# Performance work log

Hardware: AMD Instinct MI355X
Metric: run time of the kernel (lower is better)

## Reference

```python
import jax, jax.numpy as jnp
import numpy as np

N_NODES = 100000
N_EDGES = 1600000
IN_DIM = 256
OUT_DIM = 128


def setup_inputs() -> dict:
    key = jax.random.key(0)
    k1, k2, k3, k4, k5 = jax.random.split(key, 5)
    inputs = jax.random.normal(k1, (N_NODES, IN_DIM), dtype=jnp.float32)
    # xavier_uniform with relu gain, as in the torch init
    gain = float(np.sqrt(2.0))
    limit = gain * float(np.sqrt(6.0 / (IN_DIM + OUT_DIM)))
    W = jax.random.uniform(k2, (IN_DIM, OUT_DIM), dtype=jnp.float32,
                           minval=-limit, maxval=limit)
    edge_src = jax.random.randint(k3, (N_EDGES,), 0, N_NODES, dtype=jnp.int32)
    edge_dst = jax.random.randint(k4, (N_EDGES,), 0, N_NODES, dtype=jnp.int32)
    edge_val = jax.random.uniform(k5, (N_EDGES,), dtype=jnp.float32)
    return {"inputs": inputs, "W": W, "edge_src": edge_src,
            "edge_dst": edge_dst, "edge_val": edge_val}


def reference(inputs, W, edge_src, edge_dst, edge_val):
    # x = inputs @ W  (dense GEMM)
    h = inputs @ W                                  # [N, OUT_DIM]
    # adj @ h  as SpMM over COO edges: out[d] += val * h[s]
    msg = edge_val[:, None] * h[edge_src]           # [E, OUT_DIM]
    agg = jax.ops.segment_sum(msg, edge_dst, num_segments=N_NODES)
    # act = ReLU, fused with SpMM output
    return jax.nn.relu(agg)
```

## Files before the change

### kernel.cpp

```cpp
#include <hip/hip_runtime.h>
#include <hip/hip_bf16.h>

#define N_NODES 100000
#define N_EDGES 1600000
#define IN_DIM  256
#define OUT_DIM 128

#define GEMM_ROWS   64
#define GEMM_BLOCKS ((N_NODES + GEMM_ROWS - 1) / GEMM_ROWS)

#define NBUCK   196
#define BSHIFT  9
#define BCAP    10240
#define BSTRIDE 16
#define EPB     2048
#define BIN_BLOCKS ((N_EDGES + EPB - 1) / EPB)

typedef __attribute__((ext_vector_type(8))) short bf16x8;
typedef __attribute__((ext_vector_type(4))) float f32x4;

__device__ __forceinline__ ushort f2bf(float f) {
    union { float f; unsigned u; } v; v.f = f;
    unsigned r = v.u + 0x7FFF + ((v.u >> 16) & 1);
    return (ushort)(r >> 16);
}
__device__ __forceinline__ float bflo(unsigned u) {
    union { unsigned u; float f; } v; v.u = u << 16; return v.f;
}
__device__ __forceinline__ float bfhi(unsigned u) {
    union { unsigned u; float f; } v; v.u = u & 0xFFFF0000u; return v.f;
}

__global__ __launch_bounds__(256) void pack_w(const float* __restrict__ W,
                                              ushort* __restrict__ Wp) {
    const int t = blockIdx.x * 256 + threadIdx.x;
    if (t >= 4096) return;
    const int kk = t >> 9, n = (t >> 6) & 7, l = t & 63;
    const int kbase = kk * 32 + (l >> 4) * 8;
    const int col   = n * 16 + (l & 15);
    ushort* o = Wp + (size_t)t * 8;
#pragma unroll
    for (int j = 0; j < 8; ++j)
        o[j] = f2bf(W[(size_t)(kbase + j) * OUT_DIM + col]);
}

__global__ __launch_bounds__(256) void gemm_coarse(const float* __restrict__ X,
                                                   const bf16x8* __restrict__ Bp,
                                                   ushort* __restrict__ H,
                                                   const int* __restrict__ esrc,
                                                   const int* __restrict__ edst,
                                                   const float* __restrict__ eval,
                                                   int* __restrict__ bcur,
                                                   int2* __restrict__ binned) {
    __shared__ ushort xt[GEMM_ROWS * IN_DIM];

    if (blockIdx.x >= GEMM_BLOCKS) {
        int* cnt   = (int*)xt;
        int* sbase = (int*)xt + 256;
        const int blk = blockIdx.x - GEMM_BLOCKS;
        const int cb  = blk * EPB;
        const int lim = (N_EDGES - cb < EPB) ? (N_EDGES - cb) : EPB;
        const int tid = threadIdx.x;

        if (tid < NBUCK) cnt[tid] = 0;
        __syncthreads();
        for (int i = tid; i < lim; i += 256)
            atomicAdd(&cnt[edst[cb + i] >> BSHIFT], 1);
        __syncthreads();
        if (tid < NBUCK) {
            const int c = cnt[tid];
            sbase[tid] = c ? atomicAdd(&bcur[tid * BSTRIDE], c) : 0;
            cnt[tid] = 0;
        }
        __syncthreads();
        for (int i = tid; i < lim; i += 256) {
            const int d  = edst[cb + i];
            const int bb = d >> BSHIFT;
            const int pos = sbase[bb] + atomicAdd(&cnt[bb], 1);
            if (pos < BCAP) {
                int2 rec;
                rec.x = esrc[cb + i] | ((d & 511) << 20);
                rec.y = __float_as_int(eval[cb + i]);
                binned[(size_t)bb * BCAP + pos] = rec;
            }
        }
        return;
    }

    const int row0 = blockIdx.x * GEMM_ROWS;
    const int tid  = threadIdx.x;

    float4 v[16];
#pragma unroll
    for (int it = 0; it < 16; ++it) {
        const int tr = it * 4 + (tid >> 6);
        int grow = row0 + tr; if (grow >= N_NODES) grow = N_NODES - 1;
        v[it] = *reinterpret_cast<const float4*>(X + (size_t)grow * IN_DIM + (tid & 63) * 4);
    }
#pragma unroll
    for (int it = 0; it < 16; ++it) {
        const int tr = it * 4 + (tid >> 6);
        const int tc = (tid & 63) * 4;
        ushort4 b4;
        b4.x = f2bf(v[it].x); b4.y = f2bf(v[it].y);
        b4.z = f2bf(v[it].z); b4.w = f2bf(v[it].w);
        const int byte = (tr * 512 + tc * 2) ^ ((tr & 7) << 4);
        *reinterpret_cast<ushort4*>((char*)xt + byte) = b4;
    }
    __syncthreads();

    const int lane = tid & 63;
    const int wid  = tid >> 6;
    const int wr   = wid >> 1;
    const int wc   = wid & 1;
    const int rlo  = lane & 15;
    const int kseg = lane >> 4;
    const int rl0  = wr * 32 + rlo;
    const int rl1  = rl0 + 16;
    const int rxor = (rlo & 7) << 4;

    f32x4 acc[2][4] = {};

    for (int kk = 0; kk < 8; ++kk) {
        const int cb2 = (kk * 64 + kseg * 16) ^ rxor;
        const bf16x8 A0 = *reinterpret_cast<const bf16x8*>((const char*)xt + rl0 * 512 + cb2);
        const bf16x8 A1 = *reinterpret_cast<const bf16x8*>((const char*)xt + rl1 * 512 + cb2);
        const bf16x8* bbase = Bp + (size_t)(kk * 8 + wc * 4) * 64 + lane;
#pragma unroll
        for (int n = 0; n < 4; ++n) {
            const bf16x8 Bf = bbase[(size_t)n * 64];
            acc[0][n] = __builtin_amdgcn_mfma_f32_16x16x32_bf16(A0, Bf, acc[0][n], 0, 0, 0);
            acc[1][n] = __builtin_amdgcn_mfma_f32_16x16x32_bf16(A1, Bf, acc[1][n], 0, 0, 0);
        }
    }

#pragma unroll
    for (int i = 0; i < 2; ++i) {
#pragma unroll
        for (int r = 0; r < 4; ++r) {
            const int row = row0 + wr * 32 + i * 16 + kseg * 4 + r;
            if (row < N_NODES) {
#pragma unroll
                for (int n = 0; n < 4; ++n)
                    H[(size_t)row * OUT_DIM + (wc * 4 + n) * 16 + rlo] = f2bf(acc[i][n][r]);
            }
        }
    }
}

__global__ __launch_bounds__(256) void scan_buckets(const int* __restrict__ bcur,
                                                    int* __restrict__ gbase) {
    __shared__ int ws[4];
    const int tid = threadIdx.x, lane = tid & 63, wid = tid >> 6;
    const int v = (tid < NBUCK) ? bcur[tid * BSTRIDE] : 0;
    int sv = v;
#pragma unroll
    for (int d = 1; d < 64; d <<= 1) {
        const int t = __shfl_up(sv, d, 64);
        if (lane >= d) sv += t;
    }
    if (lane == 63) ws[wid] = sv;
    __syncthreads();
    int wx = 0;
#pragma unroll
    for (int w = 0; w < 4; ++w) if (w < wid) wx += ws[w];
    if (tid < NBUCK) gbase[tid] = wx + sv - v;
}

__global__ __launch_bounds__(1024) void bin_fine(const int* __restrict__ bcur,
                                                 const int* __restrict__ gbase,
                                                 const int2* __restrict__ binned,
                                                 int* __restrict__ offsets,
                                                 int2* __restrict__ recs) {
    __shared__ int nh[512];
    __shared__ int cur[512];
    __shared__ int ws[4];
    const int b   = blockIdx.x;
    const int tid = threadIdx.x, lane = tid & 63, wid = tid >> 6;
    const int node0 = b << BSHIFT;
    int nn = N_NODES - node0; if (nn > 512) nn = 512;
    int size = bcur[b * BSTRIDE]; if (size > BCAP) size = BCAP;
    const int2* in = binned + (size_t)b * BCAP;
    const int base_out = gbase[b];

    if (tid < 512) nh[tid] = 0;
    __syncthreads();
    for (int k = tid; k < size; k += 1024)
        atomicAdd(&nh[(in[k].x >> 20) & 511], 1);
    __syncthreads();

    int a0 = 0, ts = 0, sv = 0;
    if (tid < 256) {
        a0 = nh[2 * tid];
        const int a1 = nh[2 * tid + 1];
        ts = a0 + a1;
        sv = ts;
#pragma unroll
        for (int d = 1; d < 64; d <<= 1) {
            const int t = __shfl_up(sv, d, 64);
            if (lane >= d) sv += t;
        }
        if (lane == 63) ws[wid] = sv;
    }
    __syncthreads();
    if (tid < 256) {
        int wx = 0;
#pragma unroll
        for (int w = 0; w < 4; ++w) if (w < wid) wx += ws[w];
        const int ex = wx + sv - ts;
        cur[2 * tid]     = base_out + ex;
        cur[2 * tid + 1] = base_out + ex + a0;
        if (2 * tid < nn)     offsets[node0 + 2 * tid]     = base_out + ex;
        if (2 * tid + 1 < nn) offsets[node0 + 2 * tid + 1] = base_out + ex + a0;
    }
    if (b == 0 && tid == 0) offsets[N_NODES] = N_EDGES;
    __syncthreads();

    for (int k = tid; k < size; k += 1024) {
        const int2 r = in[k];
        const int pos = atomicAdd(&cur[(r.x >> 20) & 511], 1);
        int2 o; o.x = r.x & 0xFFFFF; o.y = r.y;
        recs[pos] = o;
    }
}

__global__ __launch_bounds__(256) void spmm_pull(const ushort* __restrict__ H,
                                                 const int* __restrict__ offsets,
                                                 const int2* __restrict__ recs,
                                                 float* __restrict__ out) {
    const int tid   = threadIdx.x;
    const int lane  = tid & 63;
    const int g     = lane >> 4;
    const int c     = lane & 15;
    const int gwave = blockIdx.x * 4 + (tid >> 6);
    const int node  = gwave * 4 + g;
    if (node >= N_NODES) return;

    const int beg = offsets[node];
    const int end = offsets[node + 1];

    float a0 = 0.f, a1 = 0.f, a2 = 0.f, a3 = 0.f;
    float a4 = 0.f, a5 = 0.f, a6 = 0.f, a7 = 0.f;

    int e = beg;
    for (; e + 3 < end; e += 4) {
        const int2 r0 = recs[e + 0];
        const int2 r1 = recs[e + 1];
        const int2 r2 = recs[e + 2];
        const int2 r3 = recs[e + 3];
        const uint4 h0 = *((const uint4*)(H + (size_t)r0.x * OUT_DIM) + c);
        const uint4 h1 = *((const uint4*)(H + (size_t)r1.x * OUT_DIM) + c);
        const uint4 h2 = *((const uint4*)(H + (size_t)r2.x * OUT_DIM) + c);
        const uint4 h3 = *((const uint4*)(H + (size_t)r3.x * OUT_DIM) + c);
        const float v0 = __int_as_float(r0.y), v1 = __int_as_float(r1.y);
        const float v2 = __int_as_float(r2.y), v3 = __int_as_float(r3.y);
        a0 = fmaf(v0, bflo(h0.x), a0);  a1 = fmaf(v0, bfhi(h0.x), a1);
        a2 = fmaf(v0, bflo(h0.y), a2);  a3 = fmaf(v0, bfhi(h0.y), a3);
        a4 = fmaf(v0, bflo(h0.z), a4);  a5 = fmaf(v0, bfhi(h0.z), a5);
        a6 = fmaf(v0, bflo(h0.w), a6);  a7 = fmaf(v0, bfhi(h0.w), a7);
        a0 = fmaf(v1, bflo(h1.x), a0);  a1 = fmaf(v1, bfhi(h1.x), a1);
        a2 = fmaf(v1, bflo(h1.y), a2);  a3 = fmaf(v1, bfhi(h1.y), a3);
        a4 = fmaf(v1, bflo(h1.z), a4);  a5 = fmaf(v1, bfhi(h1.z), a5);
        a6 = fmaf(v1, bflo(h1.w), a6);  a7 = fmaf(v1, bfhi(h1.w), a7);
        a0 = fmaf(v2, bflo(h2.x), a0);  a1 = fmaf(v2, bfhi(h2.x), a1);
        a2 = fmaf(v2, bflo(h2.y), a2);  a3 = fmaf(v2, bfhi(h2.y), a3);
        a4 = fmaf(v2, bflo(h2.z), a4);  a5 = fmaf(v2, bfhi(h2.z), a5);
        a6 = fmaf(v2, bflo(h2.w), a6);  a7 = fmaf(v2, bfhi(h2.w), a7);
        a0 = fmaf(v3, bflo(h3.x), a0);  a1 = fmaf(v3, bfhi(h3.x), a1);
        a2 = fmaf(v3, bflo(h3.y), a2);  a3 = fmaf(v3, bfhi(h3.y), a3);
        a4 = fmaf(v3, bflo(h3.z), a4);  a5 = fmaf(v3, bfhi(h3.z), a5);
        a6 = fmaf(v3, bflo(h3.w), a6);  a7 = fmaf(v3, bfhi(h3.w), a7);
    }
    for (; e < end; ++e) {
        const int2 r0 = recs[e];
        const float v0 = __int_as_float(r0.y);
        const uint4 h0 = *((const uint4*)(H + (size_t)r0.x * OUT_DIM) + c);
        a0 = fmaf(v0, bflo(h0.x), a0);  a1 = fmaf(v0, bfhi(h0.x), a1);
        a2 = fmaf(v0, bflo(h0.y), a2);  a3 = fmaf(v0, bfhi(h0.y), a3);
        a4 = fmaf(v0, bflo(h0.z), a4);  a5 = fmaf(v0, bfhi(h0.z), a5);
        a6 = fmaf(v0, bflo(h0.w), a6);  a7 = fmaf(v0, bfhi(h0.w), a7);
    }

    float* op = out + (size_t)node * OUT_DIM + c * 8;
    float4 o0, o1;
    o0.x = fmaxf(a0, 0.f); o0.y = fmaxf(a1, 0.f);
    o0.z = fmaxf(a2, 0.f); o0.w = fmaxf(a3, 0.f);
    o1.x = fmaxf(a4, 0.f); o1.y = fmaxf(a5, 0.f);
    o1.z = fmaxf(a6, 0.f); o1.w = fmaxf(a7, 0.f);
    *reinterpret_cast<float4*>(op)     = o0;
    *reinterpret_cast<float4*>(op + 4) = o1;
}

extern "C" void kernel_launch(void* const* d_in, const int* in_sizes, int n_in,
                              void* d_out, int out_size, void* d_ws, size_t ws_size,
                              hipStream_t stream) {
    const float* X    = (const float*)d_in[0];
    const float* W    = (const float*)d_in[1];
    const int*   esrc = (const int*)d_in[2];
    const int*   edst = (const int*)d_in[3];
    const float* eval = (const float*)d_in[4];
    float*       out  = (float*)d_out;

    char* ws = (char*)d_ws;
    ushort* Hb     = (ushort*)ws;  ws += (size_t)N_NODES * OUT_DIM * sizeof(ushort);
    ushort* Wp     = (ushort*)ws;  ws += (size_t)4096 * 8 * sizeof(ushort);
    int*    offsets= (int*)ws;     ws += (((size_t)(N_NODES + 1) * 4 + 127) & ~(size_t)127);
    int*    bcur   = (int*)ws;     ws += (size_t)NBUCK * BSTRIDE * 4;
    int*    gbase  = (int*)ws;     ws += ((NBUCK * 4 + 127) & ~127);
    int2*   binned = (int2*)ws;    ws += (size_t)NBUCK * BCAP * sizeof(int2);
    int2*   recs   = (int2*)ws;

    pack_w<<<16, 256, 0, stream>>>(W, Wp);
    hipMemsetAsync(bcur, 0, (size_t)NBUCK * BSTRIDE * 4, stream);
    gemm_coarse<<<GEMM_BLOCKS + BIN_BLOCKS, 256, 0, stream>>>(X, (const bf16x8*)Wp, Hb,
                                                              esrc, edst, eval,
                                                              bcur, binned);

    scan_buckets<<<1, 256, 0, stream>>>(bcur, gbase);
    bin_fine<<<NBUCK, 1024, 0, stream>>>(bcur, gbase, binned, offsets, recs);

    spmm_pull<<<(N_NODES + 15) / 16, 256, 0, stream>>>(Hb, offsets, recs, out);
}
```

Before: 134.2 us.

## Load GEMM input tiles directly into LDS with smaller 16-row blocks

The GEMM phase now uses 16-row tiles instead of 64, copying fp32 X rows straight into swizzled LDS via global_load_lds. The per-element bf16 conversion moves to fragment-read time, and each wave computes a 16x32 output slice. Launch bounds request higher occupancy to hide the latency of the memory-bound X stream. The trade is re-reading W fragments from global or cache four times as often, which also shifts the binning blocks' index range. Dropping the tail guard relies on N_NODES being divisible by 16.

```diff
diff --git a/kernel.cpp b/kernel.cpp
--- a/kernel.cpp
+++ b/kernel.cpp
@@ -6,8 +6,8 @@
 #define IN_DIM  256
 #define OUT_DIM 128
 
-#define GEMM_ROWS   64
-#define GEMM_BLOCKS ((N_NODES + GEMM_ROWS - 1) / GEMM_ROWS)
+#define GEMM_ROWS   16
+#define GEMM_BLOCKS (N_NODES / GEMM_ROWS)
 
 #define NBUCK   196
 #define BSHIFT  9
@@ -44,15 +44,19 @@
         o[j] = f2bf(W[(size_t)(kbase + j) * OUT_DIM + col]);
 }
 
-__global__ __launch_bounds__(256) void gemm_coarse(const float* __restrict__ X,
-                                                   const bf16x8* __restrict__ Bp,
-                                                   ushort* __restrict__ H,
-                                                   const int* __restrict__ esrc,
-                                                   const int* __restrict__ edst,
-                                                   const float* __restrict__ eval,
-                                                   int* __restrict__ bcur,
-                                                   int2* __restrict__ binned) {
-    __shared__ ushort xt[GEMM_ROWS * IN_DIM];
+__global__ __launch_bounds__(256, 8) void gemm_coarse(const float* __restrict__ X,
+                                                      const bf16x8* __restrict__ Bp,
+                                                      ushort* __restrict__ H,
+                                                      const int* __restrict__ esrc,
+                                                      const int* __restrict__ edst,
+                                                      const float* __restrict__ eval,
+                                                      int* __restrict__ bcur,
+                                                      int2* __restrict__ binned) {
+    __shared__ float xt[GEMM_ROWS * IN_DIM];
+
+    const int tid  = threadIdx.x;
+    const int lane = tid & 63;
+    const int wid  = tid >> 6;
 
     if (blockIdx.x >= GEMM_BLOCKS) {
         int* cnt   = (int*)xt;
@@ -60,7 +64,6 @@
         const int blk = blockIdx.x - GEMM_BLOCKS;
         const int cb  = blk * EPB;
         const int lim = (N_EDGES - cb < EPB) ? (N_EDGES - cb) : EPB;
-        const int tid = threadIdx.x;
 
         if (tid < NBUCK) cnt[tid] = 0;
         __syncthreads();
@@ -88,64 +91,45 @@
     }
 
     const int row0 = blockIdx.x * GEMM_ROWS;
-    const int tid  = threadIdx.x;
-
-    float4 v[16];
-#pragma unroll
-    for (int it = 0; it < 16; ++it) {
-        const int tr = it * 4 + (tid >> 6);
-        int grow = row0 + tr; if (grow >= N_NODES) grow = N_NODES - 1;
-        v[it] = *reinterpret_cast<const float4*>(X + (size_t)grow * IN_DIM + (tid & 63) * 4);
-    }
-#pragma unroll
-    for (int it = 0; it < 16; ++it) {
-        const int tr = it * 4 + (tid >> 6);
-        const int tc = (tid & 63) * 4;
-        ushort4 b4;
-        b4.x = f2bf(v[it].x); b4.y = f2bf(v[it].y);
-        b4.z = f2bf(v[it].z); b4.w = f2bf(v[it].w);
-        const int byte = (tr * 512 + tc * 2) ^ ((tr & 7) << 4);
-        *reinterpret_cast<ushort4*>((char*)xt + byte) = b4;
-    }
-    __syncthreads();
-
-    const int lane = tid & 63;
-    const int wid  = tid >> 6;
-    const int wr   = wid >> 1;
-    const int wc   = wid & 1;
+
+#pragma unroll
+    for (int i = 0; i < 4; ++i) {
+        const int row  = wid * 4 + i;
+        const int grow = row0 + row;
+        const float* gp = X + (size_t)grow * IN_DIM
+                        + (((lane * 16) ^ ((row & 7) << 4)) >> 2);
+        __builtin_amdgcn_global_load_lds(
+            (const __attribute__((address_space(1))) void*)gp,
+            (__attribute__((address_space(3))) void*)&xt[row * IN_DIM], 16, 0, 0);
+    }
+    __syncthreads();
+
     const int rlo  = lane & 15;
     const int kseg = lane >> 4;
-    const int rl0  = wr * 32 + rlo;
-    const int rl1  = rl0 + 16;
-    const int rxor = (rlo & 7) << 4;
-
-    f32x4 acc[2][4] = {};
-
+    const int sw   = (rlo & 7) << 4;
+
+    f32x4 acc[2] = {};
+    const char* rp = (const char*)xt + rlo * 1024;
+
+#pragma unroll
     for (int kk = 0; kk < 8; ++kk) {
-        const int cb2 = (kk * 64 + kseg * 16) ^ rxor;
-        const bf16x8 A0 = *reinterpret_cast<const bf16x8*>((const char*)xt + rl0 * 512 + cb2);
-        const bf16x8 A1 = *reinterpret_cast<const bf16x8*>((const char*)xt + rl1 * 512 + cb2);
-        const bf16x8* bbase = Bp + (size_t)(kk * 8 + wc * 4) * 64 + lane;
-#pragma unroll
-        for (int n = 0; n < 4; ++n) {
-            const bf16x8 Bf = bbase[(size_t)n * 64];
-            acc[0][n] = __builtin_amdgcn_mfma_f32_16x16x32_bf16(A0, Bf, acc[0][n], 0, 0, 0);
-            acc[1][n] = __builtin_amdgcn_mfma_f32_16x16x32_bf16(A1, Bf, acc[1][n], 0, 0, 0);
-        }
-    }
-
-#pragma unroll
-    for (int i = 0; i < 2; ++i) {
-#pragma unroll
-        for (int r = 0; r < 4; ++r) {
-            const int row = row0 + wr * 32 + i * 16 + kseg * 4 + r;
-            if (row < N_NODES) {
-#pragma unroll
-                for (int n = 0; n < 4; ++n)
-                    H[(size_t)row * OUT_DIM + (wc * 4 + n) * 16 + rlo] = f2bf(acc[i][n][r]);
-            }
-        }
-    }
+        const int base = kk * 128 + kseg * 32;
+        const float4 alo = *(const float4*)(rp + (base ^ sw));
+        const float4 ahi = *(const float4*)(rp + ((base + 16) ^ sw));
+        bf16x8 A;
+        A[0]=f2bf(alo.x); A[1]=f2bf(alo.y); A[2]=f2bf(alo.z); A[3]=f2bf(alo.w);
+        A[4]=f2bf(ahi.x); A[5]=f2bf(ahi.y); A[6]=f2bf(ahi.z); A[7]=f2bf(ahi.w);
+        const bf16x8* bbase = Bp + (size_t)(kk * 8 + wid * 2) * 64 + lane;
+        acc[0] = __builtin_amdgcn_mfma_f32_16x16x32_bf16(A, bbase[0],  acc[0], 0, 0, 0);
+        acc[1] = __builtin_amdgcn_mfma_f32_16x16x32_bf16(A, bbase[64], acc[1], 0, 0, 0);
+    }
+
+#pragma unroll
+    for (int n = 0; n < 2; ++n)
+#pragma unroll
+        for (int r = 0; r < 4; ++r)
+            H[(size_t)(row0 + kseg * 4 + r) * OUT_DIM + wid * 32 + n * 16 + rlo]
+                = f2bf(acc[n][r]);
 }
 
 __global__ __launch_bounds__(256) void scan_buckets(const int* __restrict__ bcur,
```

After: 140.9 us. 5.1% more time.
